# Optimization experiments

Hardware: AMD Instinct MI355X
Metric: run time of the kernel (lower is better)

Reference implementation:

```python
import jax, jax.numpy as jnp
import numpy as np

NEG_SLOPE = 0.2

def gat_layer(x, W, al, ar, src, dst, n_dst):
    # x: [Ns, Fin]; W: [Fin, H*D]; al/ar: [H, D]; src/dst: [E]
    H, D = al.shape
    h = (x @ W).reshape(-1, H, D)          # [Ns, H, D]
    h_dst = h[:n_dst]                       # dst nodes are prefix of src nodes (DGL block)
    el = (h * al).sum(-1)                   # [Ns, H]
    er = (h_dst * ar).sum(-1)               # [Nd, H]
    e = jax.nn.leaky_relu(el[src] + er[dst], NEG_SLOPE)  # [E, H]
    m = jax.ops.segment_max(e, dst, num_segments=n_dst)  # stable edge-softmax
    a = jnp.exp(e - m[dst])
    s = jax.ops.segment_sum(a, dst, num_segments=n_dst)
    alpha = a / s[dst]                      # [E, H]
    msg = h[src] * alpha[:, :, None]        # [E, H, D]
    out = jax.ops.segment_sum(msg, dst, num_segments=n_dst)  # [Nd, H, D]
    return out.reshape(n_dst, H * D)


def setup_inputs() -> dict:
    key = jax.random.key(0)
    ks = jax.random.split(key, 16)
    N0, N1, N2, N3 = 200000, 100000, 50000, 25000
    E0, E1, E2 = 1000000, 500000, 250000
    Fin, Dh, H, C = 256, 64, 3, 40
    inp = {}
    inp['x'] = jax.random.normal(ks[0], (N0, Fin), jnp.float32)
    inp['src0'] = jax.random.randint(ks[1], (E0,), 0, N0, jnp.int32)
    inp['dst0'] = jnp.sort(jax.random.randint(ks[2], (E0,), 0, N1, jnp.int32))
    inp['src1'] = jax.random.randint(ks[3], (E1,), 0, N1, jnp.int32)
    inp['dst1'] = jnp.sort(jax.random.randint(ks[4], (E1,), 0, N2, jnp.int32))
    inp['src2'] = jax.random.randint(ks[5], (E2,), 0, N2, jnp.int32)
    inp['dst2'] = jnp.sort(jax.random.randint(ks[6], (E2,), 0, N3, jnp.int32))
    sc = lambda f: np.float32(1.0 / np.sqrt(f))
    inp['W0'] = jax.random.normal(ks[7], (Fin, H * Dh), jnp.float32) * sc(Fin)
    inp['al0'] = jax.random.normal(ks[8], (H, Dh), jnp.float32) * sc(Dh)
    inp['ar0'] = jax.random.normal(ks[9], (H, Dh), jnp.float32) * sc(Dh)
    inp['W1'] = jax.random.normal(ks[10], (H * Dh, H * Dh), jnp.float32) * sc(H * Dh)
    inp['al1'] = jax.random.normal(ks[11], (H, Dh), jnp.float32) * sc(Dh)
    inp['ar1'] = jax.random.normal(ks[12], (H, Dh), jnp.float32) * sc(Dh)
    inp['W2'] = jax.random.normal(ks[13], (H * Dh, C), jnp.float32) * sc(H * Dh)
    inp['al2'] = jax.random.normal(ks[14], (1, C), jnp.float32) * sc(C)
    inp['ar2'] = jax.random.normal(ks[15], (1, C), jnp.float32) * sc(C)
    return inp


def reference(x, src0, dst0, src1, dst1, src2, dst2,
              W0, al0, ar0, W1, al1, ar1, W2, al2, ar2):
    N1, N2, N3 = 100000, 50000, 25000
    h = gat_layer(x, W0, al0, ar0, src0, dst0, N1)
    h = jax.nn.relu(h)  # dropout is identity in eval/deterministic mode
    h = gat_layer(h, W1, al1, ar1, src1, dst1, N2)
    h = jax.nn.relu(h)
    out = gat_layer(h, W2, al2, ar2, src2, dst2, N3)  # [N3, n_classes]
    return out
```

## Files before the change

### kernel.cpp

```cpp
#include <hip/hip_runtime.h>
#include <math.h>

#define DEV_INLINE __device__ __forceinline__

typedef __attribute__((ext_vector_type(8))) short short8v;
typedef __attribute__((ext_vector_type(4))) float float4v;

DEV_INLINE unsigned short f2bf_rtn(float f) {
  unsigned u = __float_as_uint(f);
  u += 0x7FFFu + ((u >> 16) & 1u);
  return (unsigned short)(u >> 16);
}
DEV_INLINE float bf2f(unsigned short s) { return __uint_as_float(((unsigned)s) << 16); }

DEV_INLINE int soff(int row, int oct) { return row * 32 + ((oct ^ ((row >> 1) & 3)) << 3); }

__global__ void conv_w_all(const float* __restrict__ W0, const float* __restrict__ W1,
                           const float* __restrict__ W2, short* __restrict__ w0h,
                           short* __restrict__ w0l, short* __restrict__ w1h,
                           short* __restrict__ w1l, short* __restrict__ w2h,
                           short* __restrict__ w2l) {
  const int S0 = 256 * 192, S1 = 192 * 192, S2 = 192 * 40;
  int idx = blockIdx.x * 256 + threadIdx.x;
  const float* W; short *Wh, *Wl; int K;
  if (idx < S0) { W = W0; Wh = w0h; Wl = w0l; K = 256; }
  else if (idx < S0 + S1) { idx -= S0; W = W1; Wh = w1h; Wl = w1l; K = 192; }
  else if (idx < S0 + S1 + S2) { idx -= S0 + S1; W = W2; Wh = w2h; Wl = w2l; K = 192; }
  else return;
  int n = idx / K, k = idx - n * K;
  int N = (W == W0 || W == W1) ? 192 : 40;
  float w = W[(size_t)k * N + n];
  unsigned short h = f2bf_rtn(w);
  Wh[idx] = (short)h;
  Wl[idx] = (short)f2bf_rtn(w - bf2f(h));
}

__global__ void csr_all(const int* __restrict__ d0, const int* __restrict__ d1,
                        const int* __restrict__ d2, int* __restrict__ o0,
                        int* __restrict__ o1, int* __restrict__ o2,
                        int E0, int E1, int E2, int n1, int n2, int n3) {
  int i = blockIdx.x * 256 + threadIdx.x;
  const int* dst; int* off; int E, nd;
  if (i < E0) { dst = d0; off = o0; E = E0; nd = n1; }
  else if (i < E0 + E1) { i -= E0; dst = d1; off = o1; E = E1; nd = n2; }
  else if (i < E0 + E1 + E2) { i -= E0 + E1; dst = d2; off = o2; E = E2; nd = n3; }
  else return;
  int d = dst[i];
  int p = (i == 0) ? -1 : dst[i - 1];
  for (int q = p + 1; q <= d; ++q) off[q] = i;
  if (i == E - 1)
    for (int q = d + 1; q <= nd; ++q) off[q] = E;
}

#define ISSUE_TILE(k0)                                                        \
  {                                                                           \
    _Pragma("unroll")                                                         \
    for (int p = 0; p < 2; ++p) {                                             \
      int gr = m0 + sr + p * 64;                                              \
      if (gr < M) {                                                           \
        const float* ap = A + (size_t)gr * K + (k0) + oct * 8;                \
        pa0[p] = *(const float4*)ap;                                          \
        pa1[p] = *(const float4*)(ap + 4);                                    \
      } else {                                                                \
        pa0[p] = make_float4(0.f, 0.f, 0.f, 0.f);                             \
        pa1[p] = pa0[p];                                                      \
      }                                                                       \
    }                                                                         \
    _Pragma("unroll")                                                         \
    for (int q = 0; q < BREP; ++q) {                                          \
      int n = sr + q * 64;                                                    \
      if (n < BN) {                                                           \
        if (n < N) {                                                          \
          pbh[q] = *(const short8v*)(Bth + (size_t)n * K + (k0) + oct * 8);   \
          pbl[q] = *(const short8v*)(Btl + (size_t)n * K + (k0) + oct * 8);   \
        } else {                                                              \
          _Pragma("unroll")                                                   \
          for (int j = 0; j < 8; ++j) { pbh[q][j] = 0; pbl[q][j] = 0; }       \
        }                                                                     \
      }                                                                       \
    }                                                                         \
  }

template <int NT, int H>
__global__ __launch_bounds__(256) void gemm_fused(
    const float* __restrict__ A, const short* __restrict__ Bth,
    const short* __restrict__ Btl, const float* __restrict__ al,
    const float* __restrict__ ar, float* __restrict__ C,
    float* __restrict__ el, float* __restrict__ er,
    int M, int N, int K, int n_dst) {
  constexpr int BN = NT * 16;
  constexpr int BREP = (BN + 63) / 64;
  constexpr int TPH = NT / H;
  __shared__ short As_h[128 * 32], As_l[128 * 32];
  __shared__ short Bs_h[BN * 32], Bs_l[BN * 32];
  const int tid = threadIdx.x;
  const int w = tid >> 6, lane = tid & 63;
  const int quad = lane >> 4, l16 = lane & 15;
  const int m0 = blockIdx.x * 128;

  float4v acc[2][NT];
#pragma unroll
  for (int mt = 0; mt < 2; ++mt)
#pragma unroll
    for (int nt = 0; nt < NT; ++nt)
#pragma unroll
      for (int r = 0; r < 4; ++r) acc[mt][nt][r] = 0.f;

  const int sr = tid >> 2;
  const int oct = tid & 3;

  float4 pa0[2], pa1[2];
  short8v pbh[BREP], pbl[BREP];

  ISSUE_TILE(0);

  const int nk = K >> 5;
  for (int kt = 0; kt < nk; ++kt) {
    __syncthreads();
#pragma unroll
    for (int p = 0; p < 2; ++p) {
      int r = sr + p * 64;
      float vs[8] = {pa0[p].x, pa0[p].y, pa0[p].z, pa0[p].w,
                     pa1[p].x, pa1[p].y, pa1[p].z, pa1[p].w};
      short8v hv, lv;
#pragma unroll
      for (int j = 0; j < 8; ++j) {
        unsigned short h = f2bf_rtn(vs[j]);
        hv[j] = (short)h;
        lv[j] = (short)f2bf_rtn(vs[j] - bf2f(h));
      }
      *(short8v*)(As_h + soff(r, oct)) = hv;
      *(short8v*)(As_l + soff(r, oct)) = lv;
    }
#pragma unroll
    for (int q = 0; q < BREP; ++q) {
      int n = sr + q * 64;
      if (n < BN) {
        *(short8v*)(Bs_h + soff(n, oct)) = pbh[q];
        *(short8v*)(Bs_l + soff(n, oct)) = pbl[q];
      }
    }
    __syncthreads();
    if (kt + 1 < nk) ISSUE_TILE((kt + 1) << 5);
    short8v afh[2], afl[2];
#pragma unroll
    for (int mt = 0; mt < 2; ++mt) {
      int row = w * 32 + mt * 16 + l16;
      afh[mt] = *(const short8v*)(As_h + soff(row, quad));
      afl[mt] = *(const short8v*)(As_l + soff(row, quad));
    }
#pragma unroll
    for (int nt = 0; nt < NT; ++nt) {
      int col = nt * 16 + l16;
      short8v bfh = *(const short8v*)(Bs_h + soff(col, quad));
      short8v bfl = *(const short8v*)(Bs_l + soff(col, quad));
#pragma unroll
      for (int mt = 0; mt < 2; ++mt) {
        acc[mt][nt] = __builtin_amdgcn_mfma_f32_16x16x32_bf16(afh[mt], bfh, acc[mt][nt], 0, 0, 0);
        acc[mt][nt] = __builtin_amdgcn_mfma_f32_16x16x32_bf16(afh[mt], bfl, acc[mt][nt], 0, 0, 0);
        acc[mt][nt] = __builtin_amdgcn_mfma_f32_16x16x32_bf16(afl[mt], bfh, acc[mt][nt], 0, 0, 0);
      }
    }
  }

  float av[NT], rv[NT];
#pragma unroll
  for (int nt = 0; nt < NT; ++nt) {
    int col = nt * 16 + l16;
    av[nt] = (col < N) ? al[col] : 0.f;
    rv[nt] = (col < N) ? ar[col] : 0.f;
  }
#pragma unroll
  for (int mt = 0; mt < 2; ++mt)
#pragma unroll
    for (int r = 0; r < 4; ++r) {
      int gm = m0 + w * 32 + mt * 16 + quad * 4 + r;
      if (gm >= M) continue;
      float pl[H], pr[H];
#pragma unroll
      for (int h = 0; h < H; ++h) { pl[h] = 0.f; pr[h] = 0.f; }
#pragma unroll
      for (int nt = 0; nt < NT; ++nt) {
        int h = nt / TPH;
        pl[h] = fmaf(acc[mt][nt][r], av[nt], pl[h]);
        pr[h] = fmaf(acc[mt][nt][r], rv[nt], pr[h]);
      }
#pragma unroll
      for (int h = 0; h < H; ++h) {
#pragma unroll
        for (int o = 8; o >= 1; o >>= 1) {
          pl[h] += __shfl_xor(pl[h], o, 16);
          pr[h] += __shfl_xor(pr[h], o, 16);
        }
      }
      if (l16 == 0) {
#pragma unroll
        for (int h = 0; h < H; ++h) {
          el[gm * H + h] = pl[h];
          if (gm < n_dst) er[gm * H + h] = pr[h];
        }
      }
#pragma unroll
      for (int nt = 0; nt < NT; ++nt) {
        int col = nt * 16 + l16;
        if (col < N) C[(size_t)gm * N + col] = acc[mt][nt][r];
      }
    }
}

template <int H, int D, bool RELU>
__global__ __launch_bounds__(256) void agg2_kernel(
    const float* __restrict__ hsrc, const float* __restrict__ el,
    const float* __restrict__ er, const int* __restrict__ src,
    const int* __restrict__ off, float* __restrict__ out, int n_dst) {
  constexpr int F = H * D;
  constexpr int NP = (F + 63) / 64;
  __shared__ float wbuf[16][16][H];
  __shared__ int sbuf[16][16];
  const int g = threadIdx.x >> 4, l = threadIdx.x & 15;
  const int d = blockIdx.x * 16 + g;
  if (d >= n_dst) return;
  const int lo = off[d], hi = off[d + 1];

  if (hi <= lo) {
#pragma unroll
    for (int p = 0; p < NP; ++p) {
      int c4 = (p * 16 + l) * 4;
      if (c4 < F) *(float4*)(out + (size_t)d * F + c4) = make_float4(0.f, 0.f, 0.f, 0.f);
    }
    return;
  }

  float erv[H], s_part[H];
#pragma unroll
  for (int h = 0; h < H; ++h) {
    erv[h] = er[d * H + h];
    s_part[h] = 0.f;
  }
  float4 acc[NP];
#pragma unroll
  for (int p = 0; p < NP; ++p) acc[p] = make_float4(0.f, 0.f, 0.f, 0.f);

  for (int base = lo; base < hi; base += 16) {
    const int i = base + l;
    const bool valid = i < hi;
    const int sid = valid ? src[i] : 0;
#pragma unroll
    for (int h = 0; h < H; ++h) {
      float e = 0.f;
      if (valid) {
        e = el[sid * H + h] + erv[h];
        e = e > 0.f ? e : 0.2f * e;
        e = __expf(e);
      }
      s_part[h] += e;
      wbuf[g][l][h] = e;
    }
    sbuf[g][l] = sid;

    const int cnt = min(16, hi - base);
    int sj = sbuf[g][0];
    float4 hv[NP], hn[NP];
#pragma unroll
    for (int p = 0; p < NP; ++p) {
      int c4 = (p * 16 + l) * 4;
      hv[p] = (c4 < F) ? *(const float4*)(hsrc + (size_t)sj * F + c4)
                       : make_float4(0.f, 0.f, 0.f, 0.f);
    }
    for (int ei = 0; ei < cnt; ++ei) {
      if (ei + 1 < cnt) {
        int sj2 = sbuf[g][ei + 1];
#pragma unroll
        for (int p = 0; p < NP; ++p) {
          int c4 = (p * 16 + l) * 4;
          hn[p] = (c4 < F) ? *(const float4*)(hsrc + (size_t)sj2 * F + c4)
                           : make_float4(0.f, 0.f, 0.f, 0.f);
        }
      }
#pragma unroll
      for (int p = 0; p < NP; ++p) {
        int c4 = (p * 16 + l) * 4;
        float wc = wbuf[g][ei][c4 / D];
        acc[p].x = fmaf(wc, hv[p].x, acc[p].x);
        acc[p].y = fmaf(wc, hv[p].y, acc[p].y);
        acc[p].z = fmaf(wc, hv[p].z, acc[p].z);
        acc[p].w = fmaf(wc, hv[p].w, acc[p].w);
      }
#pragma unroll
      for (int p = 0; p < NP; ++p) hv[p] = hn[p];
    }
  }

#pragma unroll
  for (int h = 0; h < H; ++h)
#pragma unroll
    for (int o = 8; o >= 1; o >>= 1) s_part[h] += __shfl_xor(s_part[h], o, 16);

#pragma unroll
  for (int p = 0; p < NP; ++p) {
    int c4 = (p * 16 + l) * 4;
    if (c4 < F) {
      float inv = 1.f / s_part[c4 / D];
      float4 o;
      o.x = acc[p].x * inv; o.y = acc[p].y * inv;
      o.z = acc[p].z * inv; o.w = acc[p].w * inv;
      if (RELU) {
        o.x = fmaxf(o.x, 0.f); o.y = fmaxf(o.y, 0.f);
        o.z = fmaxf(o.z, 0.f); o.w = fmaxf(o.w, 0.f);
      }
      *(float4*)(out + (size_t)d * F + c4) = o;
    }
  }
}

extern "C" void kernel_launch(void* const* d_in, const int* in_sizes, int n_in,
                              void* d_out, int out_size, void* d_ws, size_t ws_size,
                              hipStream_t stream) {
  const float* x   = (const float*)d_in[0];
  const int* src0  = (const int*)d_in[1];
  const int* dst0  = (const int*)d_in[2];
  const int* src1  = (const int*)d_in[3];
  const int* dst1  = (const int*)d_in[4];
  const int* src2  = (const int*)d_in[5];
  const int* dst2  = (const int*)d_in[6];
  const float* W0  = (const float*)d_in[7];
  const float* al0 = (const float*)d_in[8];
  const float* ar0 = (const float*)d_in[9];
  const float* W1  = (const float*)d_in[10];
  const float* al1 = (const float*)d_in[11];
  const float* ar1 = (const float*)d_in[12];
  const float* W2  = (const float*)d_in[13];
  const float* al2 = (const float*)d_in[14];
  const float* ar2 = (const float*)d_in[15];

  const int N0 = 200000, N1 = 100000, N2 = 50000, N3 = 25000;
  const int E0 = in_sizes[1], E1 = in_sizes[3], E2 = in_sizes[5];
  const int Fin = 256, F = 192, C = 40;

  float* ws     = (float*)d_ws;
  float* h_buf  = ws;
  float* o_buf  = h_buf + (size_t)N0 * F;
  float* el_buf = o_buf + (size_t)N1 * F;
  float* er_buf = el_buf + (size_t)N0 * 3;
  short* w0h    = (short*)(er_buf + (size_t)N1 * 3);
  short* w0l    = w0h + 192 * 256;
  short* w1h    = w0l + 192 * 256;
  short* w1l    = w1h + 192 * 192;
  short* w2h    = w1l + 192 * 192;
  short* w2l    = w2h + 40 * 192;
  int*   off0   = (int*)(w2l + 40 * 192);
  int*   off1   = off0 + (N1 + 1);
  int*   off2   = off1 + (N2 + 1);

  dim3 blk(256);

  const int WTOT = 256 * 192 + 192 * 192 + 192 * 40;
  conv_w_all<<<dim3((WTOT + 255) / 256), blk, 0, stream>>>(W0, W1, W2, w0h, w0l, w1h, w1l, w2h, w2l);
  const int ETOT = E0 + E1 + E2;
  csr_all<<<dim3((ETOT + 255) / 256), blk, 0, stream>>>(dst0, dst1, dst2, off0, off1, off2,
                                                        E0, E1, E2, N1, N2, N3);

  gemm_fused<12, 3><<<dim3((N0 + 127) / 128), blk, 0, stream>>>(
      x, w0h, w0l, al0, ar0, h_buf, el_buf, er_buf, N0, F, Fin, N1);
  agg2_kernel<3, 64, true><<<dim3((N1 + 15) / 16), blk, 0, stream>>>(
      h_buf, el_buf, er_buf, src0, off0, o_buf, N1);

  gemm_fused<12, 3><<<dim3((N1 + 127) / 128), blk, 0, stream>>>(
      o_buf, w1h, w1l, al1, ar1, h_buf, el_buf, er_buf, N1, F, F, N2);
  agg2_kernel<3, 64, true><<<dim3((N2 + 15) / 16), blk, 0, stream>>>(
      h_buf, el_buf, er_buf, src1, off1, o_buf, N2);

  gemm_fused<3, 1><<<dim3((N2 + 127) / 128), blk, 0, stream>>>(
      o_buf, w2h, w2l, al2, ar2, h_buf, el_buf, er_buf, N2, C, F, N3);
  agg2_kernel<1, 40, false><<<dim3((N3 + 15) / 16), blk, 0, stream>>>(
      h_buf, el_buf, er_buf, src2, off2, (float*)d_out, N3);
}
```

Measured before the change: 640.6 us.

## Load A fragments directly to registers and double-buffer B tiles in LDS

The GEMM no longer stages the A tile through shared memory. Each lane loads its own MFMA A fragment straight from global memory and splits it into bf16 hi/lo in registers. B tiles are double-buffered in LDS with a two-deep register prefetch, which leaves one barrier per k-step instead of two. The aim is to cut LDS traffic and barrier stalls, at the cost of less coalesced A loads issued in the same iteration they are consumed, so load latency is less hidden.

New measurement: 662.4 us. 1.03x slower.

```diff
diff --git a/kernel.cpp b/kernel.cpp
--- a/kernel.cpp
+++ b/kernel.cpp
@@ -52,20 +52,8 @@
     for (int q = d + 1; q <= nd; ++q) off[q] = E;
 }
 
-#define ISSUE_TILE(k0)                                                        \
+#define ISSUE_B(k0)                                                           \
   {                                                                           \
-    _Pragma("unroll")                                                         \
-    for (int p = 0; p < 2; ++p) {                                             \
-      int gr = m0 + sr + p * 64;                                              \
-      if (gr < M) {                                                           \
-        const float* ap = A + (size_t)gr * K + (k0) + oct * 8;                \
-        pa0[p] = *(const float4*)ap;                                          \
-        pa1[p] = *(const float4*)(ap + 4);                                    \
-      } else {                                                                \
-        pa0[p] = make_float4(0.f, 0.f, 0.f, 0.f);                             \
-        pa1[p] = pa0[p];                                                      \
-      }                                                                       \
-    }                                                                         \
     _Pragma("unroll")                                                         \
     for (int q = 0; q < BREP; ++q) {                                          \
       int n = sr + q * 64;                                                    \
@@ -81,6 +69,18 @@
     }                                                                         \
   }
 
+#define STAGE_B(buf)                                                          \
+  {                                                                           \
+    _Pragma("unroll")                                                         \
+    for (int q = 0; q < BREP; ++q) {                                          \
+      int n = sr + q * 64;                                                    \
+      if (n < BN) {                                                           \
+        *(short8v*)(Bs_h[buf] + soff(n, oct)) = pbh[q];                       \
+        *(short8v*)(Bs_l[buf] + soff(n, oct)) = pbl[q];                       \
+      }                                                                       \
+    }                                                                         \
+  }
+
 template <int NT, int H>
 __global__ __launch_bounds__(256) void gemm_fused(
     const float* __restrict__ A, const short* __restrict__ Bth,
@@ -91,8 +91,7 @@
   constexpr int BN = NT * 16;
   constexpr int BREP = (BN + 63) / 64;
   constexpr int TPH = NT / H;
-  __shared__ short As_h[128 * 32], As_l[128 * 32];
-  __shared__ short Bs_h[BN * 32], Bs_l[BN * 32];
+  __shared__ short Bs_h[2][BN * 32], Bs_l[2][BN * 32];
   const int tid = threadIdx.x;
   const int w = tid >> 6, lane = tid & 63;
   const int quad = lane >> 4, l16 = lane & 15;
@@ -109,51 +108,49 @@
   const int sr = tid >> 2;
   const int oct = tid & 3;
 
-  float4 pa0[2], pa1[2];
   short8v pbh[BREP], pbl[BREP];
 
-  ISSUE_TILE(0);
-
   const int nk = K >> 5;
+  ISSUE_B(0);
+  STAGE_B(0);
+  if (nk > 1) ISSUE_B(32);
+  __syncthreads();
+
   for (int kt = 0; kt < nk; ++kt) {
-    __syncthreads();
-#pragma unroll
-    for (int p = 0; p < 2; ++p) {
-      int r = sr + p * 64;
-      float vs[8] = {pa0[p].x, pa0[p].y, pa0[p].z, pa0[p].w,
-                     pa1[p].x, pa1[p].y, pa1[p].z, pa1[p].w};
-      short8v hv, lv;
+    const int cur = kt & 1;
+    const int k0 = kt << 5;
+    float4 fA[2][2];
+#pragma unroll
+    for (int mt = 0; mt < 2; ++mt) {
+      int row = m0 + w * 32 + mt * 16 + l16;
+      if (row < M) {
+        const float* ap = A + (size_t)row * K + k0 + quad * 8;
+        fA[mt][0] = *(const float4*)ap;
+        fA[mt][1] = *(const float4*)(ap + 4);
+      } else {
+        fA[mt][0] = make_float4(0.f, 0.f, 0.f, 0.f);
+        fA[mt][1] = fA[mt][0];
+      }
+    }
+    if (kt + 1 < nk) STAGE_B(cur ^ 1);
+    if (kt + 2 < nk) ISSUE_B((kt + 2) << 5);
+    short8v afh[2], afl[2];
+#pragma unroll
+    for (int mt = 0; mt < 2; ++mt) {
+      float vs[8] = {fA[mt][0].x, fA[mt][0].y, fA[mt][0].z, fA[mt][0].w,
+                     fA[mt][1].x, fA[mt][1].y, fA[mt][1].z, fA[mt][1].w};
 #pragma unroll
       for (int j = 0; j < 8; ++j) {
-        unsigned short h = f2bf_rtn(vs[j]);
-        hv[j] = (short)h;
-        lv[j] = (short)f2bf_rtn(vs[j] - bf2f(h));
-      }
-      *(short8v*)(As_h + soff(r, oct)) = hv;
-      *(short8v*)(As_l + soff(r, oct)) = lv;
-    }
-#pragma unroll
-    for (int q = 0; q < BREP; ++q) {
-      int n = sr + q * 64;
-      if (n < BN) {
-        *(short8v*)(Bs_h + soff(n, oct)) = pbh[q];
-        *(short8v*)(Bs_l + soff(n, oct)) = pbl[q];
-      }
-    }
-    __syncthreads();
-    if (kt + 1 < nk) ISSUE_TILE((kt + 1) << 5);
-    short8v afh[2], afl[2];
-#pragma unroll
-    for (int mt = 0; mt < 2; ++mt) {
-      int row = w * 32 + mt * 16 + l16;
-      afh[mt] = *(const short8v*)(As_h + soff(row, quad));
-      afl[mt] = *(const short8v*)(As_l + soff(row, quad));
+        unsigned short hh = f2bf_rtn(vs[j]);
+        afh[mt][j] = (short)hh;
+        afl[mt][j] = (short)f2bf_rtn(vs[j] - bf2f(hh));
+      }
     }
 #pragma unroll
     for (int nt = 0; nt < NT; ++nt) {
       int col = nt * 16 + l16;
-      short8v bfh = *(const short8v*)(Bs_h + soff(col, quad));
-      short8v bfl = *(const short8v*)(Bs_l + soff(col, quad));
+      short8v bfh = *(const short8v*)(Bs_h[cur] + soff(col, quad));
+      short8v bfl = *(const short8v*)(Bs_l[cur] + soff(col, quad));
 #pragma unroll
       for (int mt = 0; mt < 2; ++mt) {
         acc[mt][nt] = __builtin_amdgcn_mfma_f32_16x16x32_bf16(afh[mt], bfh, acc[mt][nt], 0, 0, 0);
@@ -161,6 +158,7 @@
         acc[mt][nt] = __builtin_amdgcn_mfma_f32_16x16x32_bf16(afl[mt], bfh, acc[mt][nt], 0, 0, 0);
       }
     }
+    if (kt + 1 < nk) __syncthreads();
   }
 
   float av[NT], rv[NT];
```
